# Kernel tuning notes

Measured on AMD Instinct MI355X. Metric: run time of the kernel, lower is better.

## Reference

```python
import jax, jax.numpy as jnp
import numpy as np

B, T, D = 2, 2048, 2048
H, K, Hd = 16, 8, 128
EPS = 1e-6
THETA = 1e6


def _rms_norm(x, w):
    # x: [..., Hd]
    return x * jax.lax.rsqrt(jnp.mean(x * x, axis=-1, keepdims=True) + EPS) * w


def _rope(x, sin, cos):
    # x: [B, T, Hh, Hd]; sin/cos: [T, Hd//2]
    s = sin[None, :, None, :]
    c = cos[None, :, None, :]
    x1 = x[..., 0::2]
    x2 = x[..., 1::2]
    # NOTE: source concatenates halves (non-interleaved output), replicate exactly
    return jnp.concatenate([x1 * c - x2 * s, x1 * s + x2 * c], axis=-1)


def setup_inputs() -> dict:
    key = jax.random.key(0)
    ks = jax.random.split(key, 5)
    scale = 0.02
    x = jax.random.normal(ks[0], (B, T, D), dtype=jnp.float32)
    Wq = jax.random.normal(ks[1], (D, H * Hd), dtype=jnp.float32) * scale
    Wk = jax.random.normal(ks[2], (D, K * Hd), dtype=jnp.float32) * scale
    Wv = jax.random.normal(ks[3], (D, K * Hd), dtype=jnp.float32) * scale
    Wo = jax.random.normal(ks[4], (H * Hd, D), dtype=jnp.float32) * scale
    qn_w = jnp.ones((Hd,), dtype=jnp.float32)
    kn_w = jnp.ones((Hd,), dtype=jnp.float32)
    # RotaryEmbedding: inv_freq = theta**(-arange(0,Hd,2)/Hd); freqs = outer(t, inv_freq)
    inv_freq = 1.0 / (THETA ** (jnp.arange(0, Hd, 2, dtype=jnp.float32) / Hd))
    freqs = jnp.arange(T, dtype=jnp.float32)[:, None] * inv_freq[None, :]
    return {"x": x, "Wq": Wq, "Wk": Wk, "Wv": Wv, "Wo": Wo,
            "qn_w": qn_w, "kn_w": kn_w,
            "sin": jnp.sin(freqs), "cos": jnp.cos(freqs)}


def reference(x, Wq, Wk, Wv, Wo, qn_w, kn_w, sin, cos):
    Bx, Tx, _ = x.shape
    q = (x @ Wq).reshape(Bx, Tx, H, Hd)
    k = (x @ Wk).reshape(Bx, Tx, K, Hd)
    v = (x @ Wv).reshape(Bx, Tx, K, Hd)
    q = _rope(_rms_norm(q, qn_w), sin, cos)
    k = _rope(_rms_norm(k, kn_w), sin, cos)
    q = q.transpose(0, 2, 1, 3)  # [B,H,T,Hd]
    k = k.transpose(0, 2, 1, 3)  # [B,K,T,Hd]
    v = v.transpose(0, 2, 1, 3)
    if K != 1 and K != H:
        rep = H // K
        k = jnp.repeat(k, rep, axis=1)  # repeat_interleave on head dim
        v = jnp.repeat(v, rep, axis=1)
    att = jnp.einsum('bhqd,bhkd->bhqk', q.astype(jnp.float32),
                     k.astype(jnp.float32)) / np.sqrt(Hd).astype(np.float32)
    causal = jnp.tril(jnp.ones((Tx, Tx), dtype=bool))
    att = jnp.where(causal[None, None], att, -jnp.inf)
    att = jax.nn.softmax(att, axis=-1)
    out = jnp.einsum('bhqk,bhkd->bhqd', att, v.astype(jnp.float32))
    out = out.astype(q.dtype).transpose(0, 2, 1, 3).reshape(Bx, Tx, H * Hd)
    return out @ Wo
```

## Files before the change

### kernel.cpp

```cpp
#include <hip/hip_runtime.h>
#include <stdint.h>


#define B_ 2
#define T_ 2048
#define D_ 2048
#define H_ 16
#define KH_ 8
#define HD_ 128
#define M_ (B_*T_)
#define NQKV_ 4096
#define QK_SCALE_LOG2E 0.1275174337f

typedef unsigned short u16;
typedef unsigned int   u32;
typedef __attribute__((ext_vector_type(8))) __bf16 bf16x8_t;
typedef __attribute__((ext_vector_type(4))) float  f32x4_t;

__device__ __forceinline__ u16 f2bf(float f) {
    u32 x = __float_as_uint(f);
    return (u16)((x + 0x7fffu + ((x >> 16) & 1u)) >> 16);
}
__device__ __forceinline__ u32 pack2(u16 a, u16 b) { return (u32)a | ((u32)b << 16); }

__device__ __forceinline__ void gload16(const void* g, void* l) {
    __builtin_amdgcn_global_load_lds(
        (__attribute__((address_space(1))) const void*)(unsigned long long)g,
        (__attribute__((address_space(3))) void*)(u32)(unsigned long long)l,
        16, 0, 0);
}

__global__ void cast_x_kernel(const float* __restrict__ in, u16* __restrict__ out) {
    int i = (blockIdx.x * 256 + threadIdx.x) * 4;
    float4 v = *(const float4*)(in + i);
    u32 lo = pack2(f2bf(v.x), f2bf(v.y));
    u32 hi = pack2(f2bf(v.z), f2bf(v.w));
    *(uint2*)(out + i) = make_uint2(lo, hi);
}

__global__ void tcast_kernel(const float* __restrict__ in, u16* __restrict__ out,
                             int ncols) {
    __shared__ u16 tile[64][65];
    int k0 = blockIdx.x * 64;
    int n0 = blockIdx.y * 64;
    int tid = threadIdx.x;
#pragma unroll
    for (int i = 0; i < 8; ++i) {
        int idx = tid + i * 256;
        int r = idx >> 5, c2 = idx & 31;
        float2 v = *(const float2*)(in + (size_t)(k0 + r) * ncols + n0 + 2 * c2);
        tile[r][2 * c2]     = f2bf(v.x);
        tile[r][2 * c2 + 1] = f2bf(v.y);
    }
    __syncthreads();
#pragma unroll
    for (int i = 0; i < 8; ++i) {
        int idx = tid + i * 256;
        int rn = idx >> 5, c2 = idx & 31;
        *(u32*)(out + (size_t)(n0 + rn) * 2048 + k0 + 2 * c2) =
            pack2(tile[2 * c2][rn], tile[2 * c2 + 1][rn]);
    }
}

__global__ void __launch_bounds__(256)
gemm_kernel(const u16* __restrict__ A, const u16* __restrict__ Bt,
            float* __restrict__ C, int N) {
    __shared__ u16 As[128 * 32];
    __shared__ u16 Bs[128 * 32];
    const int tid  = threadIdx.x;
    const int lane = tid & 63;
    const int wid  = tid >> 6;
    const int m0 = blockIdx.x * 128;
    const int n0 = blockIdx.y * 128;

    const int c0 = wid * 2, c1 = wid * 2 + 1;
    const int r0 = c0 * 16 + (lane >> 2);
    const int r1 = c1 * 16 + (lane >> 2);
    const int cl = lane & 3;
    const int g0 = cl ^ ((r0 >> 1) & 3);
    const int g1 = cl ^ ((r1 >> 1) & 3);
    const u16* gA0 = A  + (size_t)(m0 + r0) * 2048 + g0 * 8;
    const u16* gA1 = A  + (size_t)(m0 + r1) * 2048 + g1 * 8;
    const u16* gB0 = Bt + (size_t)(n0 + r0) * 2048 + g0 * 8;
    const u16* gB1 = Bt + (size_t)(n0 + r1) * 2048 + g1 * 8;
    u16* lA0 = As + c0 * 512;
    u16* lA1 = As + c1 * 512;
    u16* lB0 = Bs + c0 * 512;
    u16* lB1 = Bs + c1 * 512;

    const int wm = (wid >> 1) * 64, wn = (wid & 1) * 64;
    const int fr  = lane & 15;
    const int kg  = lane >> 4;

    f32x4_t acc[4][4];
#pragma unroll
    for (int m = 0; m < 4; ++m)
#pragma unroll
        for (int n = 0; n < 4; ++n)
#pragma unroll
            for (int j = 0; j < 4; ++j) acc[m][n][j] = 0.0f;

    for (int ks = 0; ks < 64; ++ks) {
        gload16(gA0, lA0); gload16(gA1, lA1);
        gload16(gB0, lB0); gload16(gB1, lB1);
        gA0 += 32; gA1 += 32; gB0 += 32; gB1 += 32;
        __syncthreads();
        bf16x8_t af[4], bfv[4];
#pragma unroll
        for (int m = 0; m < 4; ++m) {
            int row = wm + m * 16 + fr;
            int phys = kg ^ ((row >> 1) & 3);
            af[m] = *(const bf16x8_t*)(As + row * 32 + phys * 8);
        }
#pragma unroll
        for (int n = 0; n < 4; ++n) {
            int row = wn + n * 16 + fr;
            int phys = kg ^ ((row >> 1) & 3);
            bfv[n] = *(const bf16x8_t*)(Bs + row * 32 + phys * 8);
        }
#pragma unroll
        for (int m = 0; m < 4; ++m)
#pragma unroll
            for (int n = 0; n < 4; ++n)
                acc[m][n] = __builtin_amdgcn_mfma_f32_16x16x32_bf16(
                    af[m], bfv[n], acc[m][n], 0, 0, 0);
        __syncthreads();
    }

#pragma unroll
    for (int m = 0; m < 4; ++m)
#pragma unroll
        for (int n = 0; n < 4; ++n) {
            int col   = n0 + wn + n * 16 + fr;
            int rbase = m0 + wm + m * 16 + kg * 4;
#pragma unroll
            for (int j = 0; j < 4; ++j)
                C[(size_t)(rbase + j) * N + col] = acc[m][n][j];
        }
}

__global__ void __launch_bounds__(256)
normrope_kernel(const float* __restrict__ Cqkv,
                const float* __restrict__ qw, const float* __restrict__ kw,
                const float* __restrict__ sinT, const float* __restrict__ cosT,
                u16* __restrict__ qbf, u16* __restrict__ kbf, u16* __restrict__ vbf) {
    int lane = threadIdx.x & 63;
    int w    = threadIdx.x >> 6;
    int rid  = blockIdx.x * 4 + w;
    int m   = rid >> 5;
    int sub = rid & 31;
    int b = m >> 11, t = m & (T_ - 1);

    if (sub >= 24) {
        int kh = sub - 24;
        float2 x = *(const float2*)(Cqkv + (size_t)m * NQKV_ + 3072 + kh * HD_ + 2 * lane);
        *(u32*)(vbf + ((size_t)(b * KH_ + kh) * T_ + t) * HD_ + 2 * lane) =
            pack2(f2bf(x.x), f2bf(x.y));
        return;
    }
    bool isq = sub < 16;
    int  hh  = isq ? sub : sub - 16;
    int  colbase = isq ? hh * HD_ : 2048 + hh * HD_;
    float2 x = *(const float2*)(Cqkv + (size_t)m * NQKV_ + colbase + 2 * lane);
    float ss = x.x * x.x + x.y * x.y;
#pragma unroll
    for (int sh = 1; sh < 64; sh <<= 1) ss += __shfl_xor(ss, sh, 64);
    float scale = rsqrtf(ss * (1.0f / 128.0f) + 1e-6f);
    const float* wp = isq ? qw : kw;
    float2 wv = *(const float2*)(wp + 2 * lane);
    float y1 = x.x * scale * wv.x;
    float y2 = x.y * scale * wv.y;
    float c = cosT[t * 64 + lane], s = sinT[t * 64 + lane];
    float oa = y1 * c - y2 * s;
    float ob = y1 * s + y2 * c;
    if (isq) { oa *= QK_SCALE_LOG2E; ob *= QK_SCALE_LOG2E; }
    u16* outp = isq ? (qbf + ((size_t)(b * H_  + hh) * T_ + t) * HD_)
                    : (kbf + ((size_t)(b * KH_ + hh) * T_ + t) * HD_);
    outp[lane]      = f2bf(oa);
    outp[64 + lane] = f2bf(ob);
}

__global__ void vtrans_kernel(const u16* __restrict__ in, u16* __restrict__ out) {
    __shared__ u16 tile[64][65];
    int t0 = blockIdx.x * 64;
    int d0 = blockIdx.y * 64;
    size_t bi = (size_t)blockIdx.z * T_ * HD_;
    size_t bo = (size_t)blockIdx.z * HD_ * T_;
    int tid = threadIdx.x;
#pragma unroll
    for (int i = 0; i < 8; ++i) {
        int idx = tid + i * 256;
        int r = idx >> 5, c2 = idx & 31;
        u32 v = *(const u32*)(in + bi + (size_t)(t0 + r) * HD_ + d0 + 2 * c2);
        tile[r][2 * c2]     = (u16)(v & 0xffffu);
        tile[r][2 * c2 + 1] = (u16)(v >> 16);
    }
    __syncthreads();
#pragma unroll
    for (int i = 0; i < 8; ++i) {
        int idx = tid + i * 256;
        int rd = idx >> 5, c2 = idx & 31;
        *(u32*)(out + bo + (size_t)(d0 + rd) * T_ + t0 + 2 * c2) =
            pack2(tile[2 * c2][rd], tile[2 * c2 + 1][rd]);
    }
}

__global__ void __launch_bounds__(512)
attn_kernel(const u16* __restrict__ qg, const u16* __restrict__ kgl,
            const u16* __restrict__ vtg, u16* __restrict__ attout) {
    __shared__ u16 Kt[2][64 * 128];
    __shared__ u16 Vt[2][128 * 64];
    __shared__ u16 Pb[8][16 * 72];

    const int tid = threadIdx.x, lane = tid & 63, w = tid >> 6;
    const int qb = (int)gridDim.x - 1 - (int)blockIdx.x;
    const int h = blockIdx.y, b = blockIdx.z;
    const int kh = h >> 1;
    const int q0 = qb * 128;
    const u16* qbase = qg  + ((size_t)(b * H_  + h ) * T_) * HD_;
    const u16* kbase = kgl + ((size_t)(b * KH_ + kh) * T_) * HD_;
    const u16* vbase = vtg + ((size_t)(b * KH_ + kh) * HD_) * T_;

    const int fr  = lane & 15;
    const int kg4 = lane >> 4;
    const int qw0 = q0 + w * 16;

    bf16x8_t qf[4];
#pragma unroll
    for (int dblk = 0; dblk < 4; ++dblk)
        qf[dblk] = *(const bf16x8_t*)(qbase + (size_t)(qw0 + fr) * HD_ + dblk * 32 + kg4 * 8);

    const int krl = lane >> 4, kcl = lane & 15;
    const int vrl = lane >> 3, vcl = lane & 7;

    f32x4_t o[8];
#pragma unroll
    for (int dg = 0; dg < 8; ++dg)
#pragma unroll
        for (int j = 0; j < 4; ++j) o[dg][j] = 0.0f;
    float mrow[4], lrow[4];
#pragma unroll
    for (int j = 0; j < 4; ++j) { mrow[j] = -1e30f; lrow[j] = 0.0f; }

    const int nt = 2 * (qb + 1);

#define STAGE(buf, tt)                                                         \
    do {                                                                       \
        int kv0s = (tt) * 64;                                                  \
        if (w < 4) {                                                           \
            _Pragma("unroll")                                                  \
            for (int cc = 0; cc < 4; ++cc) {                                   \
                int c = w * 4 + cc;                                            \
                int r = c * 4 + krl;                                           \
                int g = kcl ^ (r & 7);                                         \
                gload16(kbase + (size_t)(kv0s + r) * HD_ + g * 8,              \
                        &Kt[buf][c * 512]);                                    \
            }                                                                  \
        } else {                                                               \
            _Pragma("unroll")                                                  \
            for (int cc = 0; cc < 4; ++cc) {                                   \
                int c = (w - 4) * 4 + cc;                                      \
                int rv = c * 8 + vrl;                                          \
                int gv = vcl ^ (rv & 7);                                       \
                gload16(vbase + (size_t)rv * T_ + kv0s + gv * 8,               \
                        &Vt[buf][c * 512]);                                    \
            }                                                                  \
        }                                                                      \
    } while (0)

    STAGE(0, 0);
    __syncthreads();

    for (int t = 0; t < nt; ++t) {
        const int cur = t & 1;
        const int kv0 = t * 64;
        if (t + 1 < nt) STAGE(cur ^ 1, t + 1);

        if (kv0 <= qw0 + 15) {
            f32x4_t s[4];
            __builtin_amdgcn_s_setprio(1);
#pragma unroll
            for (int cg = 0; cg < 4; ++cg) {
#pragma unroll
                for (int j = 0; j < 4; ++j) s[cg][j] = 0.0f;
#pragma unroll
                for (int dblk = 0; dblk < 4; ++dblk) {
                    int row  = cg * 16 + fr;
                    int phys = (dblk * 4 + kg4) ^ (row & 7);
                    bf16x8_t kf = *(const bf16x8_t*)(&Kt[cur][row * 128 + phys * 8]);
                    s[cg] = __builtin_amdgcn_mfma_f32_16x16x32_bf16(qf[dblk], kf, s[cg], 0, 0, 0);
                }
            }
            __builtin_amdgcn_s_setprio(0);
            if (kv0 + 63 > qw0) {
#pragma unroll
                for (int cg = 0; cg < 4; ++cg) {
                    int kv = kv0 + cg * 16 + fr;
#pragma unroll
                    for (int j = 0; j < 4; ++j) {
                        int q = qw0 + kg4 * 4 + j;
                        if (kv > q) s[cg][j] = -1e30f;
                    }
                }
            }
            float tm[4];
#pragma unroll
            for (int j = 0; j < 4; ++j)
                tm[j] = fmaxf(fmaxf(s[0][j], s[1][j]), fmaxf(s[2][j], s[3][j]));
#pragma unroll
            for (int sh = 1; sh < 16; sh <<= 1)
#pragma unroll
                for (int j = 0; j < 4; ++j)
                    tm[j] = fmaxf(tm[j], __shfl_xor(tm[j], sh, 64));
            float corr[4];
#pragma unroll
            for (int j = 0; j < 4; ++j) {
                float mnew = fmaxf(mrow[j], tm[j]);
                corr[j] = exp2f(mrow[j] - mnew);
                mrow[j] = mnew;
            }
            float pr[4][4], rs[4] = {0.f, 0.f, 0.f, 0.f};
#pragma unroll
            for (int cg = 0; cg < 4; ++cg)
#pragma unroll
                for (int j = 0; j < 4; ++j) {
                    float p = exp2f(s[cg][j] - mrow[j]);
                    pr[cg][j] = p;
                    rs[j] += p;
                }
#pragma unroll
            for (int sh = 1; sh < 16; sh <<= 1)
#pragma unroll
                for (int j = 0; j < 4; ++j) rs[j] += __shfl_xor(rs[j], sh, 64);
#pragma unroll
            for (int j = 0; j < 4; ++j) lrow[j] = lrow[j] * corr[j] + rs[j];
#pragma unroll
            for (int dg = 0; dg < 8; ++dg)
#pragma unroll
                for (int j = 0; j < 4; ++j) o[dg][j] *= corr[j];
#pragma unroll
            for (int cg = 0; cg < 4; ++cg)
#pragma unroll
                for (int j = 0; j < 4; ++j)
                    Pb[w][(kg4 * 4 + j) * 72 + cg * 16 + fr] = f2bf(pr[cg][j]);
            bf16x8_t pa[2];
#pragma unroll
            for (int kvb = 0; kvb < 2; ++kvb)
                pa[kvb] = *(const bf16x8_t*)(&Pb[w][fr * 72 + kvb * 32 + kg4 * 8]);
            __builtin_amdgcn_s_setprio(1);
#pragma unroll
            for (int dg = 0; dg < 8; ++dg) {
                int d = dg * 16 + fr;
#pragma unroll
                for (int kvb = 0; kvb < 2; ++kvb) {
                    int phys = (kvb * 4 + kg4) ^ (d & 7);
                    bf16x8_t vf = *(const bf16x8_t*)(&Vt[cur][d * 64 + phys * 8]);
                    o[dg] = __builtin_amdgcn_mfma_f32_16x16x32_bf16(pa[kvb], vf, o[dg], 0, 0, 0);
                }
            }
            __builtin_amdgcn_s_setprio(0);
        }
        __syncthreads();
    }
#undef STAGE

    float inv[4];
#pragma unroll
    for (int j = 0; j < 4; ++j) inv[j] = 1.0f / lrow[j];
    size_t rb = (size_t)(b * T_ + qw0);
#pragma unroll
    for (int dg = 0; dg < 8; ++dg)
#pragma unroll
        for (int j = 0; j < 4; ++j)
            attout[(rb + kg4 * 4 + j) * 2048 + h * HD_ + dg * 16 + fr] =
                f2bf(o[dg][j] * inv[j]);
}

extern "C" void kernel_launch(void* const* d_in, const int* in_sizes, int n_in,
                              void* d_out, int out_size, void* d_ws, size_t ws_size,
                              hipStream_t stream) {
    const float* x    = (const float*)d_in[0];
    const float* Wq   = (const float*)d_in[1];
    const float* Wk   = (const float*)d_in[2];
    const float* Wv   = (const float*)d_in[3];
    const float* Wo   = (const float*)d_in[4];
    const float* qw   = (const float*)d_in[5];
    const float* kw   = (const float*)d_in[6];
    const float* sinT = (const float*)d_in[7];
    const float* cosT = (const float*)d_in[8];
    float* out = (float*)d_out;

    u16*  x_bf   = (u16*)d_ws;
    u16*  wqkv_t = x_bf   + (size_t)M_ * D_;
    u16*  wo_t   = wqkv_t + (size_t)4096 * 2048;
    float* c_qkv = (float*)(wo_t + (size_t)2048 * 2048);
    u16*  q_bf   = (u16*)(c_qkv + (size_t)M_ * NQKV_);
    u16*  k_bf   = q_bf + (size_t)B_ * H_  * T_ * HD_;
    u16*  v_bf   = k_bf + (size_t)B_ * KH_ * T_ * HD_;
    u16*  v_t    = v_bf + (size_t)B_ * KH_ * T_ * HD_;
    u16*  att_bf = v_t  + (size_t)B_ * KH_ * T_ * HD_;

    cast_x_kernel<<<(M_ * D_) / 1024, 256, 0, stream>>>(x, x_bf);
    tcast_kernel<<<dim3(32, 32), 256, 0, stream>>>(Wq, wqkv_t, 2048);
    tcast_kernel<<<dim3(32, 16), 256, 0, stream>>>(Wk, wqkv_t + (size_t)2048 * 2048, 1024);
    tcast_kernel<<<dim3(32, 16), 256, 0, stream>>>(Wv, wqkv_t + (size_t)3072 * 2048, 1024);
    tcast_kernel<<<dim3(32, 32), 256, 0, stream>>>(Wo, wo_t, 2048);

    gemm_kernel<<<dim3(32, 32), 256, 0, stream>>>(x_bf, wqkv_t, c_qkv, 4096);
    normrope_kernel<<<(M_ * 32) / 4, 256, 0, stream>>>(c_qkv, qw, kw, sinT, cosT,
                                                       q_bf, k_bf, v_bf);
    vtrans_kernel<<<dim3(32, 2, 16), 256, 0, stream>>>(v_bf, v_t);
    attn_kernel<<<dim3(16, 16, 2), 512, 0, stream>>>(q_bf, k_bf, v_t, att_bf);
    gemm_kernel<<<dim3(32, 16), 256, 0, stream>>>(att_bf, wo_t, out, 2048);
}
```

Baseline: 478.2 us.

## Rewrite attention with 32x32x16 MFMA, transposed S, register P, 4 waves

The attention kernel moves from 16x16x32 MFMA with 8 waves of 16 query rows to 32x32x16 MFMA with 4 waves of 32 query rows. S is computed transposed (K as the A operand), so each lane owns one query column and the row max and sum need only one cross-half shuffle. P is repacked into MFMA operands with lane shuffles instead of going through a shared-memory buffer. Output goes through LDS for coalesced 16-byte stores. The goal is fewer shuffles, less LDS traffic and higher MFMA throughput, at the cost of more registers per thread and fewer waves per block.

```diff
diff --git a/kernel.cpp b/kernel.cpp
--- a/kernel.cpp
+++ b/kernel.cpp
@@ -14,8 +14,10 @@
 
 typedef unsigned short u16;
 typedef unsigned int   u32;
-typedef __attribute__((ext_vector_type(8))) __bf16 bf16x8_t;
-typedef __attribute__((ext_vector_type(4))) float  f32x4_t;
+typedef __attribute__((ext_vector_type(8)))  __bf16 bf16x8_t;
+typedef __attribute__((ext_vector_type(4)))  float  f32x4_t;
+typedef __attribute__((ext_vector_type(16))) float  f32x16_t;
+typedef __attribute__((ext_vector_type(4)))  u32    u32x4_t;
 
 __device__ __forceinline__ u16 f2bf(float f) {
     u32 x = __float_as_uint(f);
@@ -205,67 +207,58 @@
     }
 }
 
-__global__ void __launch_bounds__(512)
+__global__ void __launch_bounds__(256, 2)
 attn_kernel(const u16* __restrict__ qg, const u16* __restrict__ kgl,
             const u16* __restrict__ vtg, u16* __restrict__ attout) {
     __shared__ u16 Kt[2][64 * 128];
     __shared__ u16 Vt[2][128 * 64];
-    __shared__ u16 Pb[8][16 * 72];
 
     const int tid = threadIdx.x, lane = tid & 63, w = tid >> 6;
     const int qb = (int)gridDim.x - 1 - (int)blockIdx.x;
     const int h = blockIdx.y, b = blockIdx.z;
     const int kh = h >> 1;
     const int q0 = qb * 128;
+    const int col = lane & 31;
+    const int hi  = lane >> 5;
+    const int l7  = lane & 7;
+    const int l15 = lane & 15;
+    const int qw0 = q0 + w * 32;
+    const int qlane = qw0 + col;
+
     const u16* qbase = qg  + ((size_t)(b * H_  + h ) * T_) * HD_;
     const u16* kbase = kgl + ((size_t)(b * KH_ + kh) * T_) * HD_;
     const u16* vbase = vtg + ((size_t)(b * KH_ + kh) * HD_) * T_;
 
-    const int fr  = lane & 15;
-    const int kg4 = lane >> 4;
-    const int qw0 = q0 + w * 16;
-
-    bf16x8_t qf[4];
-#pragma unroll
-    for (int dblk = 0; dblk < 4; ++dblk)
-        qf[dblk] = *(const bf16x8_t*)(qbase + (size_t)(qw0 + fr) * HD_ + dblk * 32 + kg4 * 8);
+    bf16x8_t qf[8];
+#pragma unroll
+    for (int s = 0; s < 8; ++s)
+        qf[s] = *(const bf16x8_t*)(qbase + (size_t)qlane * HD_ + s * 16 + hi * 8);
 
     const int krl = lane >> 4, kcl = lane & 15;
     const int vrl = lane >> 3, vcl = lane & 7;
 
-    f32x4_t o[8];
-#pragma unroll
-    for (int dg = 0; dg < 8; ++dg)
-#pragma unroll
-        for (int j = 0; j < 4; ++j) o[dg][j] = 0.0f;
-    float mrow[4], lrow[4];
-#pragma unroll
-    for (int j = 0; j < 4; ++j) { mrow[j] = -1e30f; lrow[j] = 0.0f; }
+    f32x16_t o[4];
+#pragma unroll
+    for (int dt = 0; dt < 4; ++dt)
+#pragma unroll
+        for (int r = 0; r < 16; ++r) o[dt][r] = 0.0f;
+    float mrow = -1e30f, lrow = 0.0f;
 
     const int nt = 2 * (qb + 1);
 
-#define STAGE(buf, tt)                                                         \
-    do {                                                                       \
-        int kv0s = (tt) * 64;                                                  \
-        if (w < 4) {                                                           \
-            _Pragma("unroll")                                                  \
-            for (int cc = 0; cc < 4; ++cc) {                                   \
-                int c = w * 4 + cc;                                            \
-                int r = c * 4 + krl;                                           \
-                int g = kcl ^ (r & 7);                                         \
-                gload16(kbase + (size_t)(kv0s + r) * HD_ + g * 8,              \
-                        &Kt[buf][c * 512]);                                    \
-            }                                                                  \
-        } else {                                                               \
-            _Pragma("unroll")                                                  \
-            for (int cc = 0; cc < 4; ++cc) {                                   \
-                int c = (w - 4) * 4 + cc;                                      \
-                int rv = c * 8 + vrl;                                          \
-                int gv = vcl ^ (rv & 7);                                       \
-                gload16(vbase + (size_t)rv * T_ + kv0s + gv * 8,               \
-                        &Vt[buf][c * 512]);                                    \
-            }                                                                  \
-        }                                                                      \
+#define STAGE(buf, tt)                                                          \
+    do {                                                                        \
+        int kv0s = (tt) * 64;                                                   \
+        _Pragma("unroll")                                                       \
+        for (int cc = 0; cc < 4; ++cc) {                                        \
+            int c = w * 4 + cc;                                                 \
+            int r = c * 4 + krl;                                                \
+            gload16(kbase + (size_t)(kv0s + r) * HD_ + (kcl ^ (r & 15)) * 8,    \
+                    &Kt[buf][c * 512]);                                         \
+            int rv = c * 8 + vrl;                                               \
+            gload16(vbase + (size_t)rv * T_ + kv0s + (vcl ^ (rv & 7)) * 8,      \
+                    &Vt[buf][c * 512]);                                         \
+        }                                                                       \
     } while (0)
 
     STAGE(0, 0);
@@ -276,86 +269,79 @@
         const int kv0 = t * 64;
         if (t + 1 < nt) STAGE(cur ^ 1, t + 1);
 
-        if (kv0 <= qw0 + 15) {
-            f32x4_t s[4];
+        if (kv0 <= qw0 + 31) {
+            f32x16_t s0, s1;
+#pragma unroll
+            for (int r = 0; r < 16; ++r) { s0[r] = 0.0f; s1[r] = 0.0f; }
             __builtin_amdgcn_s_setprio(1);
 #pragma unroll
-            for (int cg = 0; cg < 4; ++cg) {
-#pragma unroll
-                for (int j = 0; j < 4; ++j) s[cg][j] = 0.0f;
-#pragma unroll
-                for (int dblk = 0; dblk < 4; ++dblk) {
-                    int row  = cg * 16 + fr;
-                    int phys = (dblk * 4 + kg4) ^ (row & 7);
-                    bf16x8_t kf = *(const bf16x8_t*)(&Kt[cur][row * 128 + phys * 8]);
-                    s[cg] = __builtin_amdgcn_mfma_f32_16x16x32_bf16(qf[dblk], kf, s[cg], 0, 0, 0);
-                }
+            for (int ss = 0; ss < 8; ++ss) {
+                bf16x8_t kf0 = *(const bf16x8_t*)
+                    (&Kt[cur][col * 128 + (((2 * ss + hi) ^ l15) * 8)]);
+                s0 = __builtin_amdgcn_mfma_f32_32x32x16_bf16(kf0, qf[ss], s0, 0, 0, 0);
+                bf16x8_t kf1 = *(const bf16x8_t*)
+                    (&Kt[cur][(32 + col) * 128 + (((2 * ss + hi) ^ l15) * 8)]);
+                s1 = __builtin_amdgcn_mfma_f32_32x32x16_bf16(kf1, qf[ss], s1, 0, 0, 0);
             }
             __builtin_amdgcn_s_setprio(0);
             if (kv0 + 63 > qw0) {
 #pragma unroll
-                for (int cg = 0; cg < 4; ++cg) {
-                    int kv = kv0 + cg * 16 + fr;
-#pragma unroll
-                    for (int j = 0; j < 4; ++j) {
-                        int q = qw0 + kg4 * 4 + j;
-                        if (kv > q) s[cg][j] = -1e30f;
-                    }
+                for (int r = 0; r < 16; ++r) {
+                    int cr = (r & 3) + 8 * (r >> 2) + 4 * hi;
+                    if (kv0 + cr      > qlane) s0[r] = -1e30f;
+                    if (kv0 + 32 + cr > qlane) s1[r] = -1e30f;
                 }
             }
-            float tm[4];
-#pragma unroll
-            for (int j = 0; j < 4; ++j)
-                tm[j] = fmaxf(fmaxf(s[0][j], s[1][j]), fmaxf(s[2][j], s[3][j]));
-#pragma unroll
-            for (int sh = 1; sh < 16; sh <<= 1)
-#pragma unroll
-                for (int j = 0; j < 4; ++j)
-                    tm[j] = fmaxf(tm[j], __shfl_xor(tm[j], sh, 64));
-            float corr[4];
-#pragma unroll
-            for (int j = 0; j < 4; ++j) {
-                float mnew = fmaxf(mrow[j], tm[j]);
-                corr[j] = exp2f(mrow[j] - mnew);
-                mrow[j] = mnew;
-            }
-            float pr[4][4], rs[4] = {0.f, 0.f, 0.f, 0.f};
-#pragma unroll
-            for (int cg = 0; cg < 4; ++cg)
-#pragma unroll
-                for (int j = 0; j < 4; ++j) {
-                    float p = exp2f(s[cg][j] - mrow[j]);
-                    pr[cg][j] = p;
-                    rs[j] += p;
-                }
-#pragma unroll
-            for (int sh = 1; sh < 16; sh <<= 1)
-#pragma unroll
-                for (int j = 0; j < 4; ++j) rs[j] += __shfl_xor(rs[j], sh, 64);
-#pragma unroll
-            for (int j = 0; j < 4; ++j) lrow[j] = lrow[j] * corr[j] + rs[j];
-#pragma unroll
-            for (int dg = 0; dg < 8; ++dg)
-#pragma unroll
-                for (int j = 0; j < 4; ++j) o[dg][j] *= corr[j];
-#pragma unroll
-            for (int cg = 0; cg < 4; ++cg)
-#pragma unroll
-                for (int j = 0; j < 4; ++j)
-                    Pb[w][(kg4 * 4 + j) * 72 + cg * 16 + fr] = f2bf(pr[cg][j]);
-            bf16x8_t pa[2];
-#pragma unroll
-            for (int kvb = 0; kvb < 2; ++kvb)
-                pa[kvb] = *(const bf16x8_t*)(&Pb[w][fr * 72 + kvb * 32 + kg4 * 8]);
+            float tmax = s0[0];
+#pragma unroll
+            for (int r = 1; r < 16; ++r) tmax = fmaxf(tmax, s0[r]);
+#pragma unroll
+            for (int r = 0; r < 16; ++r) tmax = fmaxf(tmax, s1[r]);
+            tmax = fmaxf(tmax, __shfl_xor(tmax, 32, 64));
+            float mnew = fmaxf(mrow, tmax);
+            float corr = exp2f(mrow - mnew);
+            mrow = mnew;
+            float ps = 0.0f;
+#pragma unroll
+            for (int r = 0; r < 16; ++r) {
+                s0[r] = exp2f(s0[r] - mrow); ps += s0[r];
+                s1[r] = exp2f(s1[r] - mrow); ps += s1[r];
+            }
+            lrow = lrow * corr + ps;
+#pragma unroll
+            for (int dt = 0; dt < 4; ++dt)
+#pragma unroll
+                for (int r = 0; r < 16; ++r) o[dt][r] *= corr;
+            u32 pd0[8], pd1[8], po0[8], po1[8];
+#pragma unroll
+            for (int i = 0; i < 8; ++i) {
+                pd0[i] = pack2(f2bf(s0[2 * i]), f2bf(s0[2 * i + 1]));
+                pd1[i] = pack2(f2bf(s1[2 * i]), f2bf(s1[2 * i + 1]));
+                po0[i] = __shfl_xor(pd0[i], 32, 64);
+                po1[i] = __shfl_xor(pd1[i], 32, 64);
+            }
+            bf16x8_t pf[4];
+#pragma unroll
+            for (int ks = 0; ks < 4; ++ks) {
+                const u32* pd = (ks < 2) ? pd0 : pd1;
+                const u32* po = (ks < 2) ? po0 : po1;
+                int base = (ks & 1) * 4;
+                union { u32 u[4]; bf16x8_t v; } f;
+                f.u[0] = hi ? po[base + 2] : pd[base + 0];
+                f.u[1] = hi ? po[base + 3] : pd[base + 1];
+                f.u[2] = hi ? pd[base + 2] : po[base + 0];
+                f.u[3] = hi ? pd[base + 3] : po[base + 1];
+                pf[ks] = f.v;
+            }
             __builtin_amdgcn_s_setprio(1);
 #pragma unroll
-            for (int dg = 0; dg < 8; ++dg) {
-                int d = dg * 16 + fr;
-#pragma unroll
-                for (int kvb = 0; kvb < 2; ++kvb) {
-                    int phys = (kvb * 4 + kg4) ^ (d & 7);
-                    bf16x8_t vf = *(const bf16x8_t*)(&Vt[cur][d * 64 + phys * 8]);
-                    o[dg] = __builtin_amdgcn_mfma_f32_16x16x32_bf16(pa[kvb], vf, o[dg], 0, 0, 0);
+            for (int dt = 0; dt < 4; ++dt) {
+                int dl = dt * 32 + col;
+#pragma unroll
+                for (int ks = 0; ks < 4; ++ks) {
+                    bf16x8_t vf = *(const bf16x8_t*)
+                        (&Vt[cur][dl * 64 + (((2 * ks + hi) ^ l7) * 8)]);
+                    o[dt] = __builtin_amdgcn_mfma_f32_32x32x16_bf16(vf, pf[ks], o[dt], 0, 0, 0);
                 }
             }
             __builtin_amdgcn_s_setprio(0);
@@ -364,16 +350,27 @@
     }
 #undef STAGE
 
-    float inv[4];
-#pragma unroll
-    for (int j = 0; j < 4; ++j) inv[j] = 1.0f / lrow[j];
-    size_t rb = (size_t)(b * T_ + qw0);
-#pragma unroll
-    for (int dg = 0; dg < 8; ++dg)
-#pragma unroll
-        for (int j = 0; j < 4; ++j)
-            attout[(rb + kg4 * 4 + j) * 2048 + h * HD_ + dg * 16 + fr] =
-                f2bf(o[dg][j] * inv[j]);
+    float ltot = lrow + __shfl_xor(lrow, 32, 64);
+    float inv  = 1.0f / ltot;
+    u16* Tr = &Kt[0][0] + w * 4096;
+#pragma unroll
+    for (int dt = 0; dt < 4; ++dt)
+#pragma unroll
+        for (int g = 0; g < 4; ++g) {
+            int slot = ((dt << 2) | g) ^ (col & 7);
+            u32 lo  = pack2(f2bf(o[dt][4 * g + 0] * inv), f2bf(o[dt][4 * g + 1] * inv));
+            u32 hi2 = pack2(f2bf(o[dt][4 * g + 2] * inv), f2bf(o[dt][4 * g + 3] * inv));
+            *(uint2*)(Tr + col * 128 + slot * 8 + 4 * hi) = make_uint2(lo, hi2);
+        }
+    size_t rowbase = (size_t)(b * T_ + qw0);
+#pragma unroll
+    for (int p = 0; p < 8; ++p) {
+        int ql   = p * 4 + (lane >> 4);
+        int slot = lane & 15;
+        int dl   = (slot ^ (ql & 7)) * 8;
+        u32x4_t v = *(const u32x4_t*)(Tr + ql * 128 + slot * 8);
+        *(u32x4_t*)(attout + (rowbase + ql) * 2048 + h * HD_ + dl) = v;
+    }
 }
 
 extern "C" void kernel_launch(void* const* d_in, const int* in_sizes, int n_in,
@@ -410,6 +407,6 @@
     normrope_kernel<<<(M_ * 32) / 4, 256, 0, stream>>>(c_qkv, qw, kw, sinT, cosT,
                                                        q_bf, k_bf, v_bf);
     vtrans_kernel<<<dim3(32, 2, 16), 256, 0, stream>>>(v_bf, v_t);
-    attn_kernel<<<dim3(16, 16, 2), 512, 0, stream>>>(q_bf, k_bf, v_t, att_bf);
+    attn_kernel<<<dim3(16, 16, 2), 256, 0, stream>>>(q_bf, k_bf, v_t, att_bf);
     gemm_kernel<<<dim3(32, 16), 256, 0, stream>>>(att_bf, wo_t, out, 2048);
 }
```

New measurement: 415.0 us. 13.2% less time.
